# Performance work log

Hardware: AMD Instinct MI355X
Metric: run time of the kernel (lower is better)

## Reference

```python
import jax, jax.numpy as jnp
import numpy as np
import math

B, T, N, D = 2, 128, 64, 128
H = 8
DK = D // H
DE = 32
LW = 8
CLIP_MIN, CLIP_MAX = -5.0, 5.0


def setup_inputs() -> dict:
    key = jax.random.key(0)
    ks = jax.random.split(key, 12)
    node = jax.random.normal(ks[0], (B, T, N, D), jnp.float32)
    tv = jax.random.normal(ks[1], (B, N, T, T, DE), jnp.float32)
    mask = jax.random.randint(ks[2], (B, 1, T), 0, 2, jnp.int32)
    # banded local mask |i-j| <= LW
    idx = jnp.arange(T)
    local_mask = (jnp.abs(idx[:, None] - idx[None, :]) <= LW).astype(jnp.float32)
    s = 0.02
    W_qkv = jax.random.normal(ks[3], (D, 3 * D), jnp.float32) * s
    b_qkv = jnp.zeros((3 * D,), jnp.float32)
    W_g = jax.random.normal(ks[4], (DE, H), jnp.float32) * s
    b_g = jnp.zeros((H,), jnp.float32)
    W_out = jax.random.normal(ks[5], (D, D), jnp.float32) * s
    b_out = jnp.zeros((D,), jnp.float32)
    W_upd = jax.random.normal(ks[6], (H, DE), jnp.float32) * s
    b_upd = jnp.zeros((DE,), jnp.float32)
    return {"node": node, "tv": tv, "mask": mask, "local_mask": local_mask,
            "W_qkv": W_qkv, "b_qkv": b_qkv, "W_g": W_g, "b_g": b_g,
            "W_out": W_out, "b_out": b_out, "W_upd": W_upd, "b_upd": b_upd}


def reference(node, tv, mask, local_mask, W_qkv, b_qkv, W_g, b_g, W_out, b_out, W_upd, b_upd):
    # node: (B,T,N,D) -> (B*N, T, D)  (einops '(b n) t d' ordering: index b*N+n)
    x = node.transpose(0, 2, 1, 3).reshape(B * N, T, D)
    qkv = x @ W_qkv + b_qkv                              # (BN, T, 3D)
    qkv = qkv.reshape(B * N, T, H, DK, 3)                # grouped (h, d_k, 3)
    q = qkv[..., 0].transpose(0, 2, 1, 3)                # (BN, H, T, DK)
    k = qkv[..., 1].transpose(0, 2, 1, 3)
    v = qkv[..., 2].transpose(0, 2, 1, 3)
    # edge-conditioned bias g: (BN, T, T, DE) -> (BN, H, T, T)
    g = (tv.reshape(B * N, T, T, DE) @ W_g + b_g).transpose(0, 3, 1, 2)
    scores = jnp.einsum('bhtd,bhsd->bhts', q, k) / math.sqrt(DK)
    scores = scores + g * local_mask                     # banded edge bias
    scores = jnp.clip(scores, CLIP_MIN, CLIP_MAX)
    m = jnp.repeat(mask, N, axis=0)[:, None]             # (BN,1,1,T)
    scores = jnp.where(m == 0, jnp.float32(1e-28), scores)
    attn = jax.nn.softmax(scores, axis=-1)
    attn = jnp.where(m == 0, jnp.float32(0.0), attn)
    xo = jnp.einsum('bhts,bhsd->bhtd', attn, v)          # (BN,H,T,DK)
    xo = xo.transpose(0, 2, 1, 3).reshape(B, N, T, D).transpose(0, 2, 1, 3)  # (B,T,N,D)
    xo = xo @ W_out + b_out
    sc = scores.reshape(B, N, H, T, T).transpose(0, 1, 3, 4, 2)  # (B,N,T,T,H)
    tv_out = sc @ W_upd + b_upd                          # (B,N,T,T,DE)
    return (xo, tv_out)
```

## Files before the change

kernel.cpp:

```cpp
#include <hip/hip_runtime.h>
#include <math.h>

#define BB 2
#define TT 128
#define NN 64
#define DD 128
#define HH 8
#define DKK 16
#define DEE 32
#define LWW 8
#define BNN (BB*NN)

__global__ __launch_bounds__(256) void qkv_kernel(
    const float* __restrict__ node, const float* __restrict__ Wqkv,
    const float* __restrict__ bqkv,
    float* __restrict__ Q, float* __restrict__ K, float* __restrict__ V) {
  __shared__ float xs[32 * 128];
  __shared__ float wl[32 * 384];
  const int tid = threadIdx.x;
  const int row0 = blockIdx.x * 32;

  {
    int i4 = tid;
    for (; i4 < 1024; i4 += 256) {
      int r = i4 >> 5, d4 = i4 & 31;
      int rowg = row0 + r;
      int bn = rowg >> 7, t = rowg & 127;
      int b = bn >> 6, n = bn & 63;
      float4 v = *(const float4*)&node[(((size_t)(b * TT + t)) * NN + n) * DD + d4 * 4];
      *(float4*)&xs[r * 128 + d4 * 4] = v;
    }
  }

  float acc[48];
#pragma unroll
  for (int i = 0; i < 48; ++i) acc[i] = 0.f;
  const int tr = tid >> 5;
  const int tc = tid & 31;

  for (int ct = 0; ct < 4; ++ct) {
    __syncthreads();
    for (int i4 = tid; i4 < 3072; i4 += 256) {
      int c = i4 / 96, j4 = i4 % 96;
      *(float4*)&wl[c * 384 + j4 * 4] =
          *(const float4*)&Wqkv[(size_t)(ct * 32 + c) * 384 + j4 * 4];
    }
    __syncthreads();
#pragma unroll 4
    for (int cl = 0; cl < 32; ++cl) {
      float xr[4];
#pragma unroll
      for (int i = 0; i < 4; ++i) xr[i] = xs[(tr * 4 + i) * 128 + ct * 32 + cl];
      float4 w0 = *(const float4*)&wl[cl * 384 + tc * 12 + 0];
      float4 w1 = *(const float4*)&wl[cl * 384 + tc * 12 + 4];
      float4 w2 = *(const float4*)&wl[cl * 384 + tc * 12 + 8];
#pragma unroll
      for (int i = 0; i < 4; ++i) {
        acc[i * 12 + 0] += xr[i] * w0.x;  acc[i * 12 + 1] += xr[i] * w0.y;
        acc[i * 12 + 2] += xr[i] * w0.z;  acc[i * 12 + 3] += xr[i] * w0.w;
        acc[i * 12 + 4] += xr[i] * w1.x;  acc[i * 12 + 5] += xr[i] * w1.y;
        acc[i * 12 + 6] += xr[i] * w1.z;  acc[i * 12 + 7] += xr[i] * w1.w;
        acc[i * 12 + 8] += xr[i] * w2.x;  acc[i * 12 + 9] += xr[i] * w2.y;
        acc[i * 12 +10] += xr[i] * w2.z;  acc[i * 12 +11] += xr[i] * w2.w;
      }
    }
  }

  const int h = tc >> 2;
  const int dk0 = (tc & 3) * 4;
#pragma unroll
  for (int i = 0; i < 4; ++i) {
    int rowg = row0 + tr * 4 + i;
    int bn = rowg >> 7, t = rowg & 127;
    float qv[4], kv[4], vv[4];
#pragma unroll
    for (int dl = 0; dl < 4; ++dl) {
      int jb = h * 48 + (dk0 + dl) * 3;
      qv[dl] = acc[i * 12 + dl * 3 + 0] + bqkv[jb + 0];
      kv[dl] = acc[i * 12 + dl * 3 + 1] + bqkv[jb + 1];
      vv[dl] = acc[i * 12 + dl * 3 + 2] + bqkv[jb + 2];
    }
    *(float4*)&Q[(size_t)rowg * 128 + h * 16 + dk0] = *(float4*)qv;
    *(float4*)&K[(((size_t)(bn * 8 + h)) * 128 + t) * 16 + dk0] = *(float4*)kv;
#pragma unroll
    for (int dl = 0; dl < 4; ++dl)
      V[(((size_t)(bn * 8 + h)) * 16 + dk0 + dl) * 128 + t] = vv[dl];
  }
}

__global__ __launch_bounds__(256) void attn_kernel(
    const float* __restrict__ Q, const float* __restrict__ K,
    const float* __restrict__ V, const float* __restrict__ tv,
    const int* __restrict__ mask,
    const float* __restrict__ Wg, const float* __restrict__ bg,
    const float* __restrict__ Wout, const float* __restrict__ bout,
    const float* __restrict__ Wupd, const float* __restrict__ bupd,
    float* __restrict__ out0, float* __restrict__ out1) {
  __shared__ float sc[8 * 8 * 128];
  __shared__ float qs[8 * 128];
  __shared__ float swg[DEE * HH];
  __shared__ float swu[HH * DEE];
  __shared__ float sbg[HH];
  __shared__ float sbu[DEE];
  __shared__ int smask[TT];

  const int tid = threadIdx.x;
  const int xcd = blockIdx.x & 7;
  const int i = blockIdx.x >> 3;
  const int bn = xcd * 16 + (i & 15);
  const int t0 = (i >> 4) * 8;
  const int b = bn >> 6, n = bn & 63;

  swg[tid & 255] = Wg[tid & 255];
  swu[tid & 255] = Wupd[tid & 255];
  if (tid < DEE) sbu[tid] = bupd[tid];
  if (tid < HH) sbg[tid] = bg[tid];
  if (tid < TT) smask[tid] = mask[b * TT + tid];
  {
    int tt = tid >> 5, d4 = tid & 31;
    *(float4*)&qs[tt * 128 + d4 * 4] =
        *(const float4*)&Q[((size_t)(bn * TT + t0 + tt)) * 128 + d4 * 4];
  }
  __syncthreads();

  for (int idx = tid; idx < HH * TT; idx += 256) {
    int h = idx >> 7, s = idx & 127;
    const float4* kp = (const float4*)&K[(((size_t)(bn * 8 + h)) * 128 + s) * 16];
    float4 k0 = kp[0], k1 = kp[1], k2 = kp[2], k3 = kp[3];
#pragma unroll
    for (int t8 = 0; t8 < 8; ++t8) {
      const float4* qp = (const float4*)&qs[t8 * 128 + h * 16];
      float4 q0 = qp[0], q1 = qp[1], q2 = qp[2], q3 = qp[3];
      float d = q0.x * k0.x + q0.y * k0.y + q0.z * k0.z + q0.w * k0.w +
                q1.x * k1.x + q1.y * k1.y + q1.z * k1.z + q1.w * k1.w +
                q2.x * k2.x + q2.y * k2.y + q2.z * k2.z + q2.w * k2.w +
                q3.x * k3.x + q3.y * k3.y + q3.z * k3.z + q3.w * k3.w;
      sc[(t8 * 8 + h) * 128 + s] = d * 0.25f;
    }
  }
  __syncthreads();

  if (tid < 8 * (2 * LWW + 1)) {
    int t8 = tid / 17, ds = tid % 17;
    int t = t0 + t8, s = t - LWW + ds;
    if (s >= 0 && s < TT) {
      const float4* tp = (const float4*)&tv[(((size_t)(bn * TT + t)) * TT + s) * DEE];
      float gh[HH];
#pragma unroll
      for (int h = 0; h < HH; ++h) gh[h] = sbg[h];
#pragma unroll
      for (int c4 = 0; c4 < 8; ++c4) {
        float4 tvv = tp[c4];
#pragma unroll
        for (int h = 0; h < HH; ++h) {
          gh[h] += tvv.x * swg[(c4 * 4 + 0) * 8 + h] +
                   tvv.y * swg[(c4 * 4 + 1) * 8 + h] +
                   tvv.z * swg[(c4 * 4 + 2) * 8 + h] +
                   tvv.w * swg[(c4 * 4 + 3) * 8 + h];
        }
      }
#pragma unroll
      for (int h = 0; h < HH; ++h) sc[(t8 * 8 + h) * 128 + s] += gh[h];
    }
  }
  __syncthreads();

  for (int idx = tid; idx < 8192; idx += 256) {
    int s = idx & 127;
    float v = sc[idx];
    v = fminf(fmaxf(v, -5.f), 5.f);
    if (smask[s] == 0) v = 1e-28f;
    sc[idx] = v;
  }
  __syncthreads();

  for (int t8 = 0; t8 < 8; ++t8) {
    int t = t0 + t8;
    float* op = out1 + (((size_t)(bn * TT + t)) * TT) * DEE;
    for (int i4 = tid; i4 < TT * DEE / 4; i4 += 256) {
      int s = i4 >> 3, e4 = i4 & 7;
      float4 o = *(const float4*)&sbu[e4 * 4];
#pragma unroll
      for (int h = 0; h < HH; ++h) {
        float f = sc[(t8 * 8 + h) * 128 + s];
        float4 w = *(const float4*)&swu[h * 32 + e4 * 4];
        o.x += f * w.x; o.y += f * w.y; o.z += f * w.z; o.w += f * w.w;
      }
      *(float4*)&op[s * DEE + e4 * 4] = o;
    }
  }
  __syncthreads();

  {
    int row = tid >> 2;
    int l4 = tid & 3;
    float* r = &sc[row * 128];
    float m = -1e30f;
#pragma unroll 8
    for (int k = 0; k < 32; ++k) m = fmaxf(m, r[l4 * 32 + k]);
    m = fmaxf(m, __shfl_xor(m, 1));
    m = fmaxf(m, __shfl_xor(m, 2));
    float ssum = 0.f;
#pragma unroll 8
    for (int k = 0; k < 32; ++k) {
      float e = __expf(r[l4 * 32 + k] - m);
      r[l4 * 32 + k] = e;
      ssum += e;
    }
    ssum += __shfl_xor(ssum, 1);
    ssum += __shfl_xor(ssum, 2);
    float inv = 1.f / ssum;
#pragma unroll 8
    for (int k = 0; k < 32; ++k) {
      int s = l4 * 32 + k;
      r[s] = (smask[s] == 0) ? 0.f : r[s] * inv;
    }
  }
  __syncthreads();

  for (int u = 0; u < 4; ++u) {
    int idx = tid + u * 256;
    int t8 = idx >> 7, hd = idx & 127;
    int h = hd >> 4, dk = hd & 15;
    const float4* vp = (const float4*)&V[(((size_t)(bn * 8 + h)) * 16 + dk) * 128];
    const float4* ap = (const float4*)&sc[(t8 * 8 + h) * 128];
    float a = 0.f;
#pragma unroll 8
    for (int s4 = 0; s4 < 32; ++s4) {
      float4 vv = vp[s4], av = ap[s4];
      a += av.x * vv.x + av.y * vv.y + av.z * vv.z + av.w * vv.w;
    }
    qs[t8 * 128 + hd] = a;
  }
  __syncthreads();

  {
    int d = tid & 127, tg = tid >> 7;
    float accp[4];
#pragma unroll
    for (int u = 0; u < 4; ++u) accp[u] = bout[d];
    for (int c = 0; c < 128; ++c) {
      float w = Wout[c * 128 + d];
#pragma unroll
      for (int u = 0; u < 4; ++u) accp[u] += qs[(tg * 4 + u) * 128 + c] * w;
    }
#pragma unroll
    for (int u = 0; u < 4; ++u) {
      int t = t0 + tg * 4 + u;
      out0[(((size_t)(b * TT + t)) * NN + n) * DD + d] = accp[u];
    }
  }
}

extern "C" void kernel_launch(void* const* d_in, const int* in_sizes, int n_in,
                              void* d_out, int out_size, void* d_ws, size_t ws_size,
                              hipStream_t stream) {
  const float* node = (const float*)d_in[0];
  const float* tv   = (const float*)d_in[1];
  const int*   mask = (const int*)d_in[2];
  const float* Wqkv = (const float*)d_in[4];
  const float* bqkv = (const float*)d_in[5];
  const float* Wg   = (const float*)d_in[6];
  const float* bg   = (const float*)d_in[7];
  const float* Wout = (const float*)d_in[8];
  const float* bout = (const float*)d_in[9];
  const float* Wupd = (const float*)d_in[10];
  const float* bupd = (const float*)d_in[11];

  float* out0 = (float*)d_out;
  float* out1 = out0 + (size_t)BB * TT * NN * DD;

  float* Q = (float*)d_ws;
  float* K = Q + (size_t)BNN * TT * DD;
  float* V = K + (size_t)BNN * TT * DD;

  qkv_kernel<<<512, 256, 0, stream>>>(node, Wqkv, bqkv, Q, K, V);
  attn_kernel<<<2048, 256, 0, stream>>>(Q, K, V, tv, mask, Wg, bg, Wout, bout,
                                        Wupd, bupd, out0, out1);
}
```

Before: 628.3 us.

## Fuse clip/mask into score passes, restructure tv_out and softmax, use nontemporal stores

Folds clipping and masking into the QK dot-product pass for off-band entries and into the edge-bias pass for in-band entries, which removes a full pass over shared scores and a barrier. The tv_out projection now keeps W_upd in registers and writes its large output with nontemporal stores. Softmax spreads each row across 32 lanes with wave shuffles, and the output projection also uses nontemporal stores. The QKV kernel halves its weight tile in shared memory, which may raise occupancy at the cost of more barriers.

```diff
diff --git a/kernel.cpp b/kernel.cpp
--- a/kernel.cpp
+++ b/kernel.cpp
@@ -11,25 +11,24 @@
 #define LWW 8
 #define BNN (BB*NN)
 
+typedef float floatx4 __attribute__((ext_vector_type(4)));
+
 __global__ __launch_bounds__(256) void qkv_kernel(
     const float* __restrict__ node, const float* __restrict__ Wqkv,
     const float* __restrict__ bqkv,
     float* __restrict__ Q, float* __restrict__ K, float* __restrict__ V) {
   __shared__ float xs[32 * 128];
-  __shared__ float wl[32 * 384];
+  __shared__ float wl[16 * 384];
   const int tid = threadIdx.x;
   const int row0 = blockIdx.x * 32;
 
-  {
-    int i4 = tid;
-    for (; i4 < 1024; i4 += 256) {
-      int r = i4 >> 5, d4 = i4 & 31;
-      int rowg = row0 + r;
-      int bn = rowg >> 7, t = rowg & 127;
-      int b = bn >> 6, n = bn & 63;
-      float4 v = *(const float4*)&node[(((size_t)(b * TT + t)) * NN + n) * DD + d4 * 4];
-      *(float4*)&xs[r * 128 + d4 * 4] = v;
-    }
+  for (int i4 = tid; i4 < 1024; i4 += 256) {
+    int r = i4 >> 5, d4 = i4 & 31;
+    int rowg = row0 + r;
+    int bn = rowg >> 7, t = rowg & 127;
+    int b = bn >> 6, n = bn & 63;
+    float4 v = *(const float4*)&node[(((size_t)(b * TT + t)) * NN + n) * DD + d4 * 4];
+    *(float4*)&xs[r * 128 + d4 * 4] = v;
   }
 
   float acc[48];
@@ -38,19 +37,19 @@
   const int tr = tid >> 5;
   const int tc = tid & 31;
 
-  for (int ct = 0; ct < 4; ++ct) {
+  for (int ct = 0; ct < 8; ++ct) {
     __syncthreads();
-    for (int i4 = tid; i4 < 3072; i4 += 256) {
+    for (int i4 = tid; i4 < 1536; i4 += 256) {
       int c = i4 / 96, j4 = i4 % 96;
       *(float4*)&wl[c * 384 + j4 * 4] =
-          *(const float4*)&Wqkv[(size_t)(ct * 32 + c) * 384 + j4 * 4];
+          *(const float4*)&Wqkv[(size_t)(ct * 16 + c) * 384 + j4 * 4];
     }
     __syncthreads();
 #pragma unroll 4
-    for (int cl = 0; cl < 32; ++cl) {
+    for (int cl = 0; cl < 16; ++cl) {
       float xr[4];
 #pragma unroll
-      for (int i = 0; i < 4; ++i) xr[i] = xs[(tr * 4 + i) * 128 + ct * 32 + cl];
+      for (int i = 0; i < 4; ++i) xr[i] = xs[(tr * 4 + i) * 128 + ct * 16 + cl];
       float4 w0 = *(const float4*)&wl[cl * 384 + tc * 12 + 0];
       float4 w1 = *(const float4*)&wl[cl * 384 + tc * 12 + 4];
       float4 w2 = *(const float4*)&wl[cl * 384 + tc * 12 + 8];
@@ -127,6 +126,7 @@
     int h = idx >> 7, s = idx & 127;
     const float4* kp = (const float4*)&K[(((size_t)(bn * 8 + h)) * 128 + s) * 16];
     float4 k0 = kp[0], k1 = kp[1], k2 = kp[2], k3 = kp[3];
+    int m0 = smask[s];
 #pragma unroll
     for (int t8 = 0; t8 < 8; ++t8) {
       const float4* qp = (const float4*)&qs[t8 * 128 + h * 16];
@@ -135,7 +135,14 @@
                 q1.x * k1.x + q1.y * k1.y + q1.z * k1.z + q1.w * k1.w +
                 q2.x * k2.x + q2.y * k2.y + q2.z * k2.z + q2.w * k2.w +
                 q3.x * k3.x + q3.y * k3.y + q3.z * k3.z + q3.w * k3.w;
-      sc[(t8 * 8 + h) * 128 + s] = d * 0.25f;
+      float v = d * 0.25f;
+      int t = t0 + t8;
+      bool inband = (s >= t - LWW) && (s <= t + LWW);
+      if (!inband) {
+        v = fminf(fmaxf(v, -5.f), 5.f);
+        if (m0 == 0) v = 1e-28f;
+      }
+      sc[(t8 * 8 + h) * 128 + s] = v;
     }
   }
   __syncthreads();
@@ -159,61 +166,71 @@
                    tvv.w * swg[(c4 * 4 + 3) * 8 + h];
         }
       }
-#pragma unroll
-      for (int h = 0; h < HH; ++h) sc[(t8 * 8 + h) * 128 + s] += gh[h];
-    }
-  }
-  __syncthreads();
-
-  for (int idx = tid; idx < 8192; idx += 256) {
-    int s = idx & 127;
-    float v = sc[idx];
-    v = fminf(fmaxf(v, -5.f), 5.f);
-    if (smask[s] == 0) v = 1e-28f;
-    sc[idx] = v;
-  }
-  __syncthreads();
-
-  for (int t8 = 0; t8 < 8; ++t8) {
-    int t = t0 + t8;
-    float* op = out1 + (((size_t)(bn * TT + t)) * TT) * DEE;
-    for (int i4 = tid; i4 < TT * DEE / 4; i4 += 256) {
-      int s = i4 >> 3, e4 = i4 & 7;
-      float4 o = *(const float4*)&sbu[e4 * 4];
+      int m0 = smask[s];
 #pragma unroll
       for (int h = 0; h < HH; ++h) {
-        float f = sc[(t8 * 8 + h) * 128 + s];
-        float4 w = *(const float4*)&swu[h * 32 + e4 * 4];
-        o.x += f * w.x; o.y += f * w.y; o.z += f * w.z; o.w += f * w.w;
-      }
-      *(float4*)&op[s * DEE + e4 * 4] = o;
-    }
-  }
-  __syncthreads();
-
-  {
-    int row = tid >> 2;
-    int l4 = tid & 3;
-    float* r = &sc[row * 128];
-    float m = -1e30f;
-#pragma unroll 8
-    for (int k = 0; k < 32; ++k) m = fmaxf(m, r[l4 * 32 + k]);
-    m = fmaxf(m, __shfl_xor(m, 1));
-    m = fmaxf(m, __shfl_xor(m, 2));
-    float ssum = 0.f;
-#pragma unroll 8
-    for (int k = 0; k < 32; ++k) {
-      float e = __expf(r[l4 * 32 + k] - m);
-      r[l4 * 32 + k] = e;
-      ssum += e;
-    }
-    ssum += __shfl_xor(ssum, 1);
-    ssum += __shfl_xor(ssum, 2);
-    float inv = 1.f / ssum;
-#pragma unroll 8
-    for (int k = 0; k < 32; ++k) {
-      int s = l4 * 32 + k;
-      r[s] = (smask[s] == 0) ? 0.f : r[s] * inv;
+        float v = sc[(t8 * 8 + h) * 128 + s] + gh[h];
+        v = fminf(fmaxf(v, -5.f), 5.f);
+        if (m0 == 0) v = 1e-28f;
+        sc[(t8 * 8 + h) * 128 + s] = v;
+      }
+    }
+  }
+  __syncthreads();
+
+  {
+    const int e4 = tid & 7;
+    const int s0 = tid >> 3;
+    float4 w[HH];
+#pragma unroll
+    for (int h = 0; h < HH; ++h) w[h] = *(const float4*)&swu[h * 32 + e4 * 4];
+    float4 bu = *(const float4*)&sbu[e4 * 4];
+    for (int t8 = 0; t8 < 8; ++t8) {
+      float* op = out1 + (((size_t)(bn * TT + t0 + t8)) * TT) * DEE;
+#pragma unroll
+      for (int si = 0; si < 4; ++si) {
+        int s = s0 + si * 32;
+        float4 o = bu;
+#pragma unroll
+        for (int h = 0; h < HH; ++h) {
+          float f = sc[(t8 * 8 + h) * 128 + s];
+          o.x += f * w[h].x; o.y += f * w[h].y;
+          o.z += f * w[h].z; o.w += f * w[h].w;
+        }
+        floatx4 ov; ov.x = o.x; ov.y = o.y; ov.z = o.z; ov.w = o.w;
+        __builtin_nontemporal_store(ov, (floatx4*)&op[s * DEE + e4 * 4]);
+      }
+    }
+  }
+  __syncthreads();
+
+  {
+    const int l = tid & 31;
+    const int rsub = tid >> 5;
+#pragma unroll
+    for (int p = 0; p < 8; ++p) {
+      int row = p * 8 + rsub;
+      float* r = &sc[row * 128];
+      float x0 = r[l], x1 = r[l + 32], x2 = r[l + 64], x3 = r[l + 96];
+      float m = fmaxf(fmaxf(x0, x1), fmaxf(x2, x3));
+      m = fmaxf(m, __shfl_xor(m, 1));
+      m = fmaxf(m, __shfl_xor(m, 2));
+      m = fmaxf(m, __shfl_xor(m, 4));
+      m = fmaxf(m, __shfl_xor(m, 8));
+      m = fmaxf(m, __shfl_xor(m, 16));
+      float e0 = __expf(x0 - m), e1 = __expf(x1 - m),
+            e2 = __expf(x2 - m), e3 = __expf(x3 - m);
+      float ssum = e0 + e1 + e2 + e3;
+      ssum += __shfl_xor(ssum, 1);
+      ssum += __shfl_xor(ssum, 2);
+      ssum += __shfl_xor(ssum, 4);
+      ssum += __shfl_xor(ssum, 8);
+      ssum += __shfl_xor(ssum, 16);
+      float inv = 1.f / ssum;
+      r[l]      = (smask[l]      == 0) ? 0.f : e0 * inv;
+      r[l + 32] = (smask[l + 32] == 0) ? 0.f : e1 * inv;
+      r[l + 64] = (smask[l + 64] == 0) ? 0.f : e2 * inv;
+      r[l + 96] = (smask[l + 96] == 0) ? 0.f : e3 * inv;
     }
   }
   __syncthreads();
@@ -247,7 +264,8 @@
 #pragma unroll
     for (int u = 0; u < 4; ++u) {
       int t = t0 + tg * 4 + u;
-      out0[(((size_t)(b * TT + t)) * NN + n) * DD + d] = accp[u];
+      __builtin_nontemporal_store(accp[u],
+          &out0[(((size_t)(b * TT + t)) * NN + n) * DD + d]);
     }
   }
 }
```

After: 576.9 us. -8.2%, faster.
